# Optimization experiments

Measured on AMD Instinct MI355X. Metric: run time of the kernel, lower is better.

Reference implementation:

```python
import jax, jax.numpy as jnp
import numpy as np

K = 5        # kernel_size
S = 1        # stride_size
EPS = 1e-5   # LayerNorm eps (torch default)


def setup_inputs() -> dict:
    key = jax.random.key(0)
    ks = jax.random.split(key, 5)
    N, C, H, W = 8, 512, 32, 32
    O = 512
    x = jax.random.normal(ks[0], (N, C, H, W), dtype=jnp.float32)
    # Linear params (torch.nn.Linear style: y = x @ W.T + b)
    proj_w = jax.random.normal(ks[1], (O, C), dtype=jnp.float32) / np.sqrt(C)
    proj_b = jax.random.normal(ks[2], (O,), dtype=jnp.float32) * 0.01
    score_w = jax.random.normal(ks[3], (1, C), dtype=jnp.float32) / np.sqrt(C)
    score_b = jax.random.normal(ks[4], (1,), dtype=jnp.float32) * 0.01
    # LayerNorm([k*k, 1]) affine params (default init: ones / zeros)
    ln_w = jnp.ones((K * K, 1), dtype=jnp.float32)
    ln_b = jnp.zeros((K * K, 1), dtype=jnp.float32)
    return {"x": x, "proj_w": proj_w, "proj_b": proj_b,
            "score_w": score_w, "score_b": score_b,
            "ln_w": ln_w, "ln_b": ln_b}


def reference(x, proj_w, proj_b, score_w, score_b, ln_w, ln_b):
    N, C, H, W = x.shape
    O = proj_w.shape[0]
    # torch does reshape (NOT permute) from [N,C,H,W] -> [N,H,W,C]
    xr = x.reshape(N, H, W, C)
    proj = xr @ proj_w.T + proj_b          # [N,H,W,O]
    score = xr @ score_w.T + score_b       # [N,H,W,1]

    Hh = (H - K) // S + 1
    Ww = (W - K) // S + 1
    ri = (jnp.arange(Hh) * S)[:, None] + jnp.arange(K)   # [Hh,K]
    ci = (jnp.arange(Ww) * S)[:, None] + jnp.arange(K)   # [Ww,K]
    # im2col-style gather of all windows at once
    p = proj[:, ri[:, None, :, None], ci[None, :, None, :], :]   # [N,Hh,Ww,K,K,O]
    p = p.reshape(N, Hh, Ww, K * K, O)
    sc = score[:, ri[:, None, :, None], ci[None, :, None, :], :] # [N,Hh,Ww,K,K,1]
    sc = sc.reshape(N, Hh, Ww, K * K, 1)

    # LayerNorm over normalized_shape=[K*K, 1] (last two axes)
    mu = jnp.mean(sc, axis=(-2, -1), keepdims=True)
    var = jnp.var(sc, axis=(-2, -1), keepdims=True)
    scn = (sc - mu) * jax.lax.rsqrt(var + EPS) * ln_w + ln_b

    w_attn = jax.nn.softmax(scn, axis=-2)                # softmax over K*K axis
    out = jnp.sum(p * w_attn, axis=-2)                   # [N,Hh,Ww,O]
    # torch stacking order yields [N, O, Hh, Ww]
    return jnp.transpose(out, (0, 3, 1, 2))
```

## Files before the change

kernel.cpp:

```cpp
#include <hip/hip_runtime.h>

typedef __bf16 bf16_t;
typedef bf16_t bf16x8 __attribute__((ext_vector_type(8)));
typedef float  f32x4  __attribute__((ext_vector_type(4)));

#define GAS __attribute__((address_space(1)))
#define LAS __attribute__((address_space(3)))

static constexpr int Nn = 8, Cc = 512, Hi = 32, Wi = 32, Oo = 512;
static constexpr int HO = 28, WO = 28;
static constexpr int NPOS = HO * WO;
static constexpr int M_ROWS = Nn * Hi * Wi;

__device__ __forceinline__ float bf2f(unsigned short u) {
  union { unsigned int i; float f; } v; v.i = ((unsigned int)u) << 16; return v.f;
}
__device__ __forceinline__ unsigned short f2bf(float f) {
  union { float f; unsigned int u; } v; v.f = f;
  unsigned int u = v.u;
  return (unsigned short)((u + 0x7fffu + ((u >> 16) & 1u)) >> 16);
}
__device__ __forceinline__ uint4 pack8(float4 f0, float4 f1) {
  uint4 r;
  r.x = (unsigned)f2bf(f0.x) | ((unsigned)f2bf(f0.y) << 16);
  r.y = (unsigned)f2bf(f0.z) | ((unsigned)f2bf(f0.w) << 16);
  r.z = (unsigned)f2bf(f1.x) | ((unsigned)f2bf(f1.y) << 16);
  r.w = (unsigned)f2bf(f1.z) | ((unsigned)f2bf(f1.w) << 16);
  return r;
}

__global__ __launch_bounds__(256) void prep_kern(
    const float* __restrict__ X, const float* __restrict__ Wf,
    const float* __restrict__ Sw, const float* __restrict__ Sb,
    unsigned short* __restrict__ Xb, unsigned short* __restrict__ Wb,
    float* __restrict__ S)
{
  const int lane = threadIdx.x & 63;
  const int wave = threadIdx.x >> 6;
  const int bid  = blockIdx.x;
  if (bid < M_ROWS / 4) {
    const int m = bid * 4 + wave;
    const float* xf = X + (size_t)m * Cc + lane * 8;
    const float4 x0 = *(const float4*)xf, x1 = *(const float4*)(xf + 4);
    *(uint4*)(Xb + (size_t)m * Cc + lane * 8) = pack8(x0, x1);
    const float* wf = Sw + lane * 8;
    const float4 w0 = *(const float4*)wf, w1 = *(const float4*)(wf + 4);
    float s = x0.x * w0.x + x0.y * w0.y + x0.z * w0.z + x0.w * w0.w
            + x1.x * w1.x + x1.y * w1.y + x1.z * w1.z + x1.w * w1.w;
    #pragma unroll
    for (int off = 32; off > 0; off >>= 1) s += __shfl_down(s, off, 64);
    if (lane == 0) S[m] = s + Sb[0];
  } else {
    const int r = (bid - M_ROWS / 4) * 4 + wave;
    const float* wf = Wf + (size_t)r * Cc + lane * 8;
    const float4 f0 = *(const float4*)wf, f1 = *(const float4*)(wf + 4);
    *(uint4*)(Wb + (size_t)r * Cc + lane * 8) = pack8(f0, f1);
  }
}

#define BM 128
#define BN 64
#define BK 32

__global__ __launch_bounds__(256) void gemm_proj(
    const bf16_t* __restrict__ Xb, const bf16_t* __restrict__ Wb,
    const float* __restrict__ Bp, unsigned short* __restrict__ P)
{
  __shared__ bf16_t lA[BM * BK];
  __shared__ bf16_t lB[BN * BK];
  const int t    = threadIdx.x;
  const int bm   = blockIdx.x;
  const int bn   = blockIdx.y;
  const int lane = t & 63;
  const int wave = t >> 6;
  const int wm   = (wave >> 1) * 64;
  const int wn   = (wave & 1) * 32;

  f32x4 acc[4][2];
  #pragma unroll
  for (int a = 0; a < 4; a++)
    #pragma unroll
    for (int b = 0; b < 2; b++) acc[a][b] = (f32x4){0.f, 0.f, 0.f, 0.f};

  const int r0 = t >> 2;
  const int c0 = (t & 3) * 8;
  const bf16_t* Ag = Xb + (size_t)(bm * BM + r0) * Cc + c0;
  const bf16_t* Bg = Wb + (size_t)(bn * BN + r0) * Cc + c0;

  for (int k0 = 0; k0 < Cc; k0 += BK) {
    __syncthreads();
    __builtin_amdgcn_global_load_lds((const GAS void*)(Ag + k0),           (LAS void*)&lA[t * 8],         16, 0, 0);
    __builtin_amdgcn_global_load_lds((const GAS void*)(Ag + 64 * Cc + k0), (LAS void*)&lA[(t + 256) * 8], 16, 0, 0);
    __builtin_amdgcn_global_load_lds((const GAS void*)(Bg + k0),           (LAS void*)&lB[t * 8],         16, 0, 0);
    __syncthreads();

    const int kof = (lane >> 4) * 8;
    bf16x8 af[4], bfr[2];
    #pragma unroll
    for (int mt = 0; mt < 4; mt++)
      af[mt] = *(const bf16x8*)&lA[(wm + mt * 16 + (lane & 15)) * BK + kof];
    #pragma unroll
    for (int nt = 0; nt < 2; nt++)
      bfr[nt] = *(const bf16x8*)&lB[(wn + nt * 16 + (lane & 15)) * BK + kof];
    #pragma unroll
    for (int mt = 0; mt < 4; mt++)
      #pragma unroll
      for (int nt = 0; nt < 2; nt++)
        acc[mt][nt] = __builtin_amdgcn_mfma_f32_16x16x32_bf16(af[mt], bfr[nt], acc[mt][nt], 0, 0, 0);
  }

  #pragma unroll
  for (int nt = 0; nt < 2; nt++) {
    const int col = bn * BN + wn + nt * 16 + (lane & 15);
    const float bias = Bp[col];
    #pragma unroll
    for (int mt = 0; mt < 4; mt++) {
      #pragma unroll
      for (int r = 0; r < 4; r++) {
        const int row = bm * BM + wm + mt * 16 + (lane >> 4) * 4 + r;
        P[(size_t)row * Oo + col] = f2bf(acc[mt][nt][r] + bias);
      }
    }
  }
}

__global__ __launch_bounds__(256) void combine_kern(
    const unsigned short* __restrict__ P, const float* __restrict__ S,
    const float* __restrict__ lnw, const float* __restrict__ lnb,
    float* __restrict__ out)
{
  const int g = blockIdx.x;
  const int n = blockIdx.y;
  const int t = threadIdx.x;
  const int ch0 = g * 16;

  __shared__ unsigned short Pt[Hi * Wi * 16];
  __shared__ float sl[Hi * Wi];
  __shared__ float lwv[25], lbv[25];

  const unsigned short* Pg = P + (size_t)n * Hi * Wi * Oo + ch0;
  #pragma unroll
  for (int itr = 0; itr < 8; itr++) {
    const int id = itr * 256 + t;
    const int row = id >> 1, half = id & 1;
    __builtin_amdgcn_global_load_lds((const GAS void*)(Pg + row * Oo + half * 8),
                                     (LAS void*)&Pt[id * 8], 16, 0, 0);
  }
  #pragma unroll
  for (int k = 0; k < 4; k++) sl[k * 256 + t] = S[n * Hi * Wi + k * 256 + t];
  if (t < 25) { lwv[t] = lnw[t]; lbv[t] = lnb[t]; }
  __syncthreads();

  for (int itp = 0; itp < 4; itp++) {
    const int pos = itp * 256 + t;
    if (pos < NPOS) {
      const int i = pos / WO;
      const int j = pos - i * WO;

      float v[25], mu = 0.f;
      #pragma unroll
      for (int q = 0; q < 25; q++) { v[q] = sl[(i + q / 5) * Wi + j + q % 5]; mu += v[q]; }
      mu *= (1.0f / 25.0f);
      float var = 0.f;
      #pragma unroll
      for (int q = 0; q < 25; q++) { const float d = v[q] - mu; var += d * d; }
      var *= (1.0f / 25.0f);
      const float rr = rsqrtf(var + 1e-5f);
      float mx = -1e30f;
      #pragma unroll
      for (int q = 0; q < 25; q++) { v[q] = (v[q] - mu) * rr * lwv[q] + lbv[q]; mx = fmaxf(mx, v[q]); }
      float den = 0.f;
      #pragma unroll
      for (int q = 0; q < 25; q++) { v[q] = __expf(v[q] - mx); den += v[q]; }
      const float inv = 1.0f / den;
      #pragma unroll
      for (int q = 0; q < 25; q++) v[q] *= inv;

      float acc[16];
      #pragma unroll
      for (int c = 0; c < 16; c++) acc[c] = 0.f;
      #pragma unroll
      for (int ki = 0; ki < 5; ki++) {
        const int rb = (i + ki) * Wi + j;
        #pragma unroll
        for (int kj = 0; kj < 5; kj++) {
          const uint4* pr = (const uint4*)&Pt[(rb + kj) * 16];
          const uint4 a = pr[0], b = pr[1];
          const float wv = v[ki * 5 + kj];
          acc[0]  += bf2f((unsigned short)(a.x & 0xFFFFu)) * wv;
          acc[1]  += bf2f((unsigned short)(a.x >> 16)) * wv;
          acc[2]  += bf2f((unsigned short)(a.y & 0xFFFFu)) * wv;
          acc[3]  += bf2f((unsigned short)(a.y >> 16)) * wv;
          acc[4]  += bf2f((unsigned short)(a.z & 0xFFFFu)) * wv;
          acc[5]  += bf2f((unsigned short)(a.z >> 16)) * wv;
          acc[6]  += bf2f((unsigned short)(a.w & 0xFFFFu)) * wv;
          acc[7]  += bf2f((unsigned short)(a.w >> 16)) * wv;
          acc[8]  += bf2f((unsigned short)(b.x & 0xFFFFu)) * wv;
          acc[9]  += bf2f((unsigned short)(b.x >> 16)) * wv;
          acc[10] += bf2f((unsigned short)(b.y & 0xFFFFu)) * wv;
          acc[11] += bf2f((unsigned short)(b.y >> 16)) * wv;
          acc[12] += bf2f((unsigned short)(b.z & 0xFFFFu)) * wv;
          acc[13] += bf2f((unsigned short)(b.z >> 16)) * wv;
          acc[14] += bf2f((unsigned short)(b.w & 0xFFFFu)) * wv;
          acc[15] += bf2f((unsigned short)(b.w >> 16)) * wv;
        }
      }
      float* og = out + ((size_t)n * Oo + ch0) * NPOS + pos;
      #pragma unroll
      for (int c = 0; c < 16; c++) og[(size_t)c * NPOS] = acc[c];
    }
  }
}

extern "C" void kernel_launch(void* const* d_in, const int* in_sizes, int n_in,
                              void* d_out, int out_size, void* d_ws, size_t ws_size,
                              hipStream_t stream) {
  const float* x   = (const float*)d_in[0];
  const float* pw  = (const float*)d_in[1];
  const float* pb  = (const float*)d_in[2];
  const float* sw  = (const float*)d_in[3];
  const float* sb  = (const float*)d_in[4];
  const float* lnw = (const float*)d_in[5];
  const float* lnb = (const float*)d_in[6];

  char* w = (char*)d_ws;
  float*          Sv = (float*)w;
  unsigned short* Xb = (unsigned short*)(w + (64 << 10));
  unsigned short* Wb = (unsigned short*)(w + (64 << 10) + (8 << 20));
  unsigned short* P  = (unsigned short*)(w + (64 << 10) + (8 << 20) + (512 << 10));

  prep_kern<<<dim3(M_ROWS / 4 + Oo / 4), 256, 0, stream>>>(x, pw, sw, sb, Xb, Wb, Sv);
  gemm_proj<<<dim3(M_ROWS / BM, Oo / BN), 256, 0, stream>>>((const bf16_t*)Xb, (const bf16_t*)Wb, pb, P);
  combine_kern<<<dim3(Oo / 16, Nn), 256, 0, stream>>>(P, Sv, lnw, lnb, (float*)d_out);
}
```

Baseline: 109.0 us.

## Apply attention pooling to inputs before projection GEMM

Because softmax weights sum to one, the weighted window sum commutes with the linear projection. The kernel now pools x windows first (using 512 input channels) and then runs the GEMM on 6272 pooled rows instead of 8192 full rows, adding the bias after. This removes the bf16 copy of X and the separate projection intermediate, and shrinks GEMM M by about a quarter. The pooled intermediate is stored as bf16, which adds a rounding step before the GEMM, and the output store becomes a vectorized float4 write in NCHW order.

```diff
diff --git a/kernel.cpp b/kernel.cpp
--- a/kernel.cpp
+++ b/kernel.cpp
@@ -10,6 +10,7 @@
 static constexpr int Nn = 8, Cc = 512, Hi = 32, Wi = 32, Oo = 512;
 static constexpr int HO = 28, WO = 28;
 static constexpr int NPOS = HO * WO;
+static constexpr int MY = Nn * NPOS;
 static constexpr int M_ROWS = Nn * Hi * Wi;
 
 __device__ __forceinline__ float bf2f(unsigned short u) {
@@ -32,8 +33,7 @@
 __global__ __launch_bounds__(256) void prep_kern(
     const float* __restrict__ X, const float* __restrict__ Wf,
     const float* __restrict__ Sw, const float* __restrict__ Sb,
-    unsigned short* __restrict__ Xb, unsigned short* __restrict__ Wb,
-    float* __restrict__ S)
+    unsigned short* __restrict__ Wb, float* __restrict__ S)
 {
   const int lane = threadIdx.x & 63;
   const int wave = threadIdx.x >> 6;
@@ -42,7 +42,6 @@
     const int m = bid * 4 + wave;
     const float* xf = X + (size_t)m * Cc + lane * 8;
     const float4 x0 = *(const float4*)xf, x1 = *(const float4*)(xf + 4);
-    *(uint4*)(Xb + (size_t)m * Cc + lane * 8) = pack8(x0, x1);
     const float* wf = Sw + lane * 8;
     const float4 w0 = *(const float4*)wf, w1 = *(const float4*)(wf + 4);
     float s = x0.x * w0.x + x0.y * w0.y + x0.z * w0.z + x0.w * w0.w
@@ -58,93 +57,26 @@
   }
 }
 
-#define BM 128
-#define BN 64
-#define BK 32
-
-__global__ __launch_bounds__(256) void gemm_proj(
-    const bf16_t* __restrict__ Xb, const bf16_t* __restrict__ Wb,
-    const float* __restrict__ Bp, unsigned short* __restrict__ P)
-{
-  __shared__ bf16_t lA[BM * BK];
-  __shared__ bf16_t lB[BN * BK];
-  const int t    = threadIdx.x;
-  const int bm   = blockIdx.x;
-  const int bn   = blockIdx.y;
-  const int lane = t & 63;
-  const int wave = t >> 6;
-  const int wm   = (wave >> 1) * 64;
-  const int wn   = (wave & 1) * 32;
-
-  f32x4 acc[4][2];
-  #pragma unroll
-  for (int a = 0; a < 4; a++)
-    #pragma unroll
-    for (int b = 0; b < 2; b++) acc[a][b] = (f32x4){0.f, 0.f, 0.f, 0.f};
-
-  const int r0 = t >> 2;
-  const int c0 = (t & 3) * 8;
-  const bf16_t* Ag = Xb + (size_t)(bm * BM + r0) * Cc + c0;
-  const bf16_t* Bg = Wb + (size_t)(bn * BN + r0) * Cc + c0;
-
-  for (int k0 = 0; k0 < Cc; k0 += BK) {
-    __syncthreads();
-    __builtin_amdgcn_global_load_lds((const GAS void*)(Ag + k0),           (LAS void*)&lA[t * 8],         16, 0, 0);
-    __builtin_amdgcn_global_load_lds((const GAS void*)(Ag + 64 * Cc + k0), (LAS void*)&lA[(t + 256) * 8], 16, 0, 0);
-    __builtin_amdgcn_global_load_lds((const GAS void*)(Bg + k0),           (LAS void*)&lB[t * 8],         16, 0, 0);
-    __syncthreads();
-
-    const int kof = (lane >> 4) * 8;
-    bf16x8 af[4], bfr[2];
-    #pragma unroll
-    for (int mt = 0; mt < 4; mt++)
-      af[mt] = *(const bf16x8*)&lA[(wm + mt * 16 + (lane & 15)) * BK + kof];
-    #pragma unroll
-    for (int nt = 0; nt < 2; nt++)
-      bfr[nt] = *(const bf16x8*)&lB[(wn + nt * 16 + (lane & 15)) * BK + kof];
-    #pragma unroll
-    for (int mt = 0; mt < 4; mt++)
-      #pragma unroll
-      for (int nt = 0; nt < 2; nt++)
-        acc[mt][nt] = __builtin_amdgcn_mfma_f32_16x16x32_bf16(af[mt], bfr[nt], acc[mt][nt], 0, 0, 0);
-  }
-
-  #pragma unroll
-  for (int nt = 0; nt < 2; nt++) {
-    const int col = bn * BN + wn + nt * 16 + (lane & 15);
-    const float bias = Bp[col];
-    #pragma unroll
-    for (int mt = 0; mt < 4; mt++) {
-      #pragma unroll
-      for (int r = 0; r < 4; r++) {
-        const int row = bm * BM + wm + mt * 16 + (lane >> 4) * 4 + r;
-        P[(size_t)row * Oo + col] = f2bf(acc[mt][nt][r] + bias);
-      }
-    }
-  }
-}
-
-__global__ __launch_bounds__(256) void combine_kern(
-    const unsigned short* __restrict__ P, const float* __restrict__ S,
+__global__ __launch_bounds__(256) void attnY_kern(
+    const float* __restrict__ X, const float* __restrict__ S,
     const float* __restrict__ lnw, const float* __restrict__ lnb,
-    float* __restrict__ out)
+    unsigned short* __restrict__ Yt)
 {
   const int g = blockIdx.x;
   const int n = blockIdx.y;
   const int t = threadIdx.x;
-  const int ch0 = g * 16;
-
-  __shared__ unsigned short Pt[Hi * Wi * 16];
+
+  __shared__ unsigned short Xt[Hi * Wi * 16];
   __shared__ float sl[Hi * Wi];
   __shared__ float lwv[25], lbv[25];
 
-  const unsigned short* Pg = P + (size_t)n * Hi * Wi * Oo + ch0;
   #pragma unroll
   for (int itr = 0; itr < 8; itr++) {
     const int id = itr * 256 + t;
-    const int row = id >> 1, half = id & 1;
-    __builtin_amdgcn_global_load_lds((const GAS void*)(Pg + row * Oo + half * 8),
-                                     (LAS void*)&Pt[id * 8], 16, 0, 0);
+    const int row = id >> 1, ch8 = (id & 1) * 8;
+    const float* xp = X + ((size_t)n * Hi * Wi + row) * Cc + g * 16 + ch8;
+    const float4 f0 = *(const float4*)xp, f1 = *(const float4*)(xp + 4);
+    *(uint4*)&Xt[row * 16 + ch8] = pack8(f0, f1);
   }
   #pragma unroll
   for (int k = 0; k < 4; k++) sl[k * 256 + t] = S[n * Hi * Wi + k * 256 + t];
@@ -173,8 +105,6 @@
       #pragma unroll
       for (int q = 0; q < 25; q++) { v[q] = __expf(v[q] - mx); den += v[q]; }
       const float inv = 1.0f / den;
-      #pragma unroll
-      for (int q = 0; q < 25; q++) v[q] *= inv;
 
       float acc[16];
       #pragma unroll
@@ -184,9 +114,9 @@
         const int rb = (i + ki) * Wi + j;
         #pragma unroll
         for (int kj = 0; kj < 5; kj++) {
-          const uint4* pr = (const uint4*)&Pt[(rb + kj) * 16];
+          const uint4* pr = (const uint4*)&Xt[(rb + kj) * 16];
           const uint4 a = pr[0], b = pr[1];
-          const float wv = v[ki * 5 + kj];
+          const float wv = v[ki * 5 + kj] * inv;
           acc[0]  += bf2f((unsigned short)(a.x & 0xFFFFu)) * wv;
           acc[1]  += bf2f((unsigned short)(a.x >> 16)) * wv;
           acc[2]  += bf2f((unsigned short)(a.y & 0xFFFFu)) * wv;
@@ -205,9 +135,90 @@
           acc[15] += bf2f((unsigned short)(b.w >> 16)) * wv;
         }
       }
-      float* og = out + ((size_t)n * Oo + ch0) * NPOS + pos;
-      #pragma unroll
-      for (int c = 0; c < 16; c++) og[(size_t)c * NPOS] = acc[c];
+      unsigned short* yp = Yt + ((size_t)g * MY + n * NPOS + pos) * 16;
+      uint4 o0, o1;
+      o0.x = (unsigned)f2bf(acc[0])  | ((unsigned)f2bf(acc[1])  << 16);
+      o0.y = (unsigned)f2bf(acc[2])  | ((unsigned)f2bf(acc[3])  << 16);
+      o0.z = (unsigned)f2bf(acc[4])  | ((unsigned)f2bf(acc[5])  << 16);
+      o0.w = (unsigned)f2bf(acc[6])  | ((unsigned)f2bf(acc[7])  << 16);
+      o1.x = (unsigned)f2bf(acc[8])  | ((unsigned)f2bf(acc[9])  << 16);
+      o1.y = (unsigned)f2bf(acc[10]) | ((unsigned)f2bf(acc[11]) << 16);
+      o1.z = (unsigned)f2bf(acc[12]) | ((unsigned)f2bf(acc[13]) << 16);
+      o1.w = (unsigned)f2bf(acc[14]) | ((unsigned)f2bf(acc[15]) << 16);
+      *(uint4*)yp = o0;
+      *(uint4*)(yp + 8) = o1;
+    }
+  }
+}
+
+#define BM 128
+#define BN 64
+#define BK 32
+
+__global__ __launch_bounds__(256) void gemm_out(
+    const unsigned short* __restrict__ Yt, const bf16_t* __restrict__ Wb,
+    const float* __restrict__ Bp, float* __restrict__ out)
+{
+  __shared__ bf16_t lA[BM * BK];
+  __shared__ bf16_t lB[BN * BK];
+  const int t    = threadIdx.x;
+  const int bm   = blockIdx.x;
+  const int bn   = blockIdx.y;
+  const int lane = t & 63;
+  const int wave = t >> 6;
+  const int wm   = (wave >> 1) * 64;
+  const int wn   = (wave & 1) * 32;
+
+  f32x4 acc[4][2];
+  #pragma unroll
+  for (int a = 0; a < 4; a++)
+    #pragma unroll
+    for (int b = 0; b < 2; b++) acc[a][b] = (f32x4){0.f, 0.f, 0.f, 0.f};
+
+  const int r0 = t >> 2;
+  const int c0 = (t & 3) * 8;
+  const int rrA = bm * BM + r0;
+  const bf16_t* Bg = Wb + (size_t)(bn * BN + r0) * Cc + c0;
+
+  for (int k0 = 0; k0 < Cc; k0 += BK) {
+    const int kk = k0 + c0;
+    const unsigned short* Ag0 = Yt + ((size_t)(kk >> 4) * MY + rrA) * 16 + (kk & 15);
+    __syncthreads();
+    __builtin_amdgcn_global_load_lds((const GAS void*)Ag0,              (LAS void*)&lA[t * 8],         16, 0, 0);
+    __builtin_amdgcn_global_load_lds((const GAS void*)(Ag0 + 64 * 16),  (LAS void*)&lA[(t + 256) * 8], 16, 0, 0);
+    __builtin_amdgcn_global_load_lds((const GAS void*)(Bg + k0),        (LAS void*)&lB[t * 8],         16, 0, 0);
+    __syncthreads();
+
+    const int kof = (lane >> 4) * 8;
+    bf16x8 af[4], bfr[2];
+    #pragma unroll
+    for (int mt = 0; mt < 4; mt++)
+      af[mt] = *(const bf16x8*)&lA[(wm + mt * 16 + (lane & 15)) * BK + kof];
+    #pragma unroll
+    for (int nt = 0; nt < 2; nt++)
+      bfr[nt] = *(const bf16x8*)&lB[(wn + nt * 16 + (lane & 15)) * BK + kof];
+    #pragma unroll
+    for (int mt = 0; mt < 4; mt++)
+      #pragma unroll
+      for (int nt = 0; nt < 2; nt++)
+        acc[mt][nt] = __builtin_amdgcn_mfma_f32_16x16x32_bf16(af[mt], bfr[nt], acc[mt][nt], 0, 0, 0);
+  }
+
+  #pragma unroll
+  for (int nt = 0; nt < 2; nt++) {
+    const int col = bn * BN + wn + nt * 16 + (lane & 15);
+    const float bias = Bp[col];
+    #pragma unroll
+    for (int mt = 0; mt < 4; mt++) {
+      const int rr0 = bm * BM + wm + mt * 16 + (lane >> 4) * 4;
+      const int n0  = rr0 / NPOS;
+      const int pos0 = rr0 - n0 * NPOS;
+      float4 q;
+      q.x = acc[mt][nt][0] + bias;
+      q.y = acc[mt][nt][1] + bias;
+      q.z = acc[mt][nt][2] + bias;
+      q.w = acc[mt][nt][3] + bias;
+      *(float4*)&out[((size_t)n0 * Oo + col) * NPOS + pos0] = q;
     }
   }
 }
@@ -225,11 +236,10 @@
 
   char* w = (char*)d_ws;
   float*          Sv = (float*)w;
-  unsigned short* Xb = (unsigned short*)(w + (64 << 10));
-  unsigned short* Wb = (unsigned short*)(w + (64 << 10) + (8 << 20));
-  unsigned short* P  = (unsigned short*)(w + (64 << 10) + (8 << 20) + (512 << 10));
-
-  prep_kern<<<dim3(M_ROWS / 4 + Oo / 4), 256, 0, stream>>>(x, pw, sw, sb, Xb, Wb, Sv);
-  gemm_proj<<<dim3(M_ROWS / BM, Oo / BN), 256, 0, stream>>>((const bf16_t*)Xb, (const bf16_t*)Wb, pb, P);
-  combine_kern<<<dim3(Oo / 16, Nn), 256, 0, stream>>>(P, Sv, lnw, lnb, (float*)d_out);
-}
+  unsigned short* Wb = (unsigned short*)(w + (64 << 10));
+  unsigned short* Yt = (unsigned short*)(w + (1 << 20));
+
+  prep_kern<<<dim3(M_ROWS / 4 + Oo / 4), 256, 0, stream>>>(x, pw, sw, sb, Wb, Sv);
+  attnY_kern<<<dim3(Oo / 16, Nn), 256, 0, stream>>>(x, Sv, lnw, lnb, Yt);
+  gemm_out<<<dim3(MY / BM, Oo / BN), 256, 0, stream>>>(Yt, (const bf16_t*)Wb, pb, (float*)d_out);
+}
```

Result: no change. 109.4 us (+0.4%).
